# Optimization experiments

Hardware: AMD Instinct MI355X
Metric: run time of the kernel (lower is better)

## Reference

```python
import jax, jax.numpy as jnp
import numpy as np

SCALE = 0.125  # 1/sqrt(embed_dim=64), as passed to Self_Attn in the original


def setup_inputs() -> dict:
    key = jax.random.key(0)
    ks = jax.random.split(key, 6)
    B, S, N, D = 8192, 50, 100000, 64
    nodes = jax.random.randint(ks[0], (B,), 0, N)
    node_seq = jax.random.randint(ks[1], (B, S), 0, N)
    uv2e_weight = jax.random.normal(ks[2], (N, D), dtype=jnp.float32)
    feat_weight = jax.random.normal(ks[3], (N, D), dtype=jnp.float32)
    W1 = jax.random.normal(ks[4], (D, 2 * D), dtype=jnp.float32) * 0.05  # torch Linear weight (out, in)
    b1 = jax.random.normal(ks[5], (D,), dtype=jnp.float32) * 0.05
    return {"nodes": nodes, "node_seq": node_seq, "uv2e_weight": uv2e_weight,
            "feat_weight": feat_weight, "W1": W1, "b1": b1}


def reference(nodes, node_seq, uv2e_weight, feat_weight, W1, b1):
    # gather embeddings: q from self ids, k=v from padded/reversed neighbor sequences
    q = uv2e_weight[nodes]          # [B, D]
    k = uv2e_weight[node_seq]       # [B, S, D]
    v = k                           # same gather in the original
    # Self_Attn: scaled dot-product attention, query length 1 per node
    scores = jnp.einsum('bd,bsd->bs', q, k) * SCALE          # [B, S]
    attn = jax.nn.softmax(scores, axis=-1)                   # [B, S]
    folded = jnp.einsum('bs,bsd->bd', attn, v)                # [B, D]
    # self features (features(nodes).t() in torch yields [B, D])
    self_feats = feat_weight[nodes]                           # [B, D]
    combined = jnp.concatenate([self_feats, folded], axis=1)  # [B, 2D]
    out = jax.nn.relu(combined @ W1.T + b1)                   # [B, D]
    return out
```

## Files before the change

kernel.cpp:

```cpp
#include <hip/hip_runtime.h>
#include <hip/hip_bf16.h>
#include <math.h>


#define DD   64
#define SS   50
#define RPW  4
#define WPB  4
#define RPB  (RPW * WPB)
#define SCALE 0.125f

__device__ __forceinline__ float rdlane_f(float v, int l) {
    return __int_as_float(__builtin_amdgcn_readlane(__float_as_int(v), l));
}

__global__ __launch_bounds__(256) void folded_encoder_kernel(
    const int*   __restrict__ nodes,
    const int*   __restrict__ node_seq,
    const float* __restrict__ uv2e,
    const float* __restrict__ feat,
    const float* __restrict__ W1,
    const float* __restrict__ b1,
    float*       __restrict__ out,
    int B)
{
    __shared__ __align__(16) float Wsw[DD][2 * DD];
    __shared__ int seqbuf[WPB][RPW * SS];

    const int tid = threadIdx.x;
    const int wid = tid >> 6;
    const int ln  = tid & 63;
    const int rr  = ln >> 4;
    const int t   = ln & 15;

    #pragma unroll
    for (int rep = 0; rep < 32; ++rep) {
        int e = rep * 256 + tid;
        int o = e >> 7;
        int i = e & 127;
        int c = i >> 2, j = i & 3;
        Wsw[o][(((c ^ (o & 7)) << 2) + j)] = W1[e];
    }

    const float bias = b1[ln];

    const int wrow0 = (blockIdx.x * WPB + wid) * RPW;

    #pragma unroll
    for (int rep = 0; rep < 4; ++rep) {
        int pos = rep * 64 + ln;
        if (pos < RPW * SS) {
            long g = (long)wrow0 * SS + pos;
            if (g < (long)B * SS) seqbuf[wid][pos] = node_seq[g];
        }
    }
    __syncthreads();

    const int row  = wrow0 + rr;
    const int rowc = row < B ? row : B - 1;
    const int nid  = nodes[rowc];

    const float4 q4 = *(const float4*)(uv2e + (size_t)nid * DD + 4 * t);
    const float4 f4 = *(const float4*)(feat + (size_t)nid * DD + 4 * t);

    const int* sb = &seqbuf[wid][rr * SS];

    float m = -INFINITY, l = 0.f;
    float4 acc = make_float4(0.f, 0.f, 0.f, 0.f);

    int    idxq[8];
    float4 kq[6];

    #pragma unroll
    for (int v = 0; v < 8; ++v) idxq[v] = sb[v];
    #pragma unroll
    for (int v = 0; v < 6; ++v)
        kq[v] = *(const float4*)(uv2e + (size_t)idxq[v] * DD + 4 * t);

    #pragma unroll
    for (int s = 0; s < SS; ++s) {
        float4 kk = kq[s % 6];
        if (s + 8 < SS) idxq[(s + 8) % 8] = sb[s + 8];
        if (s + 6 < SS)
            kq[s % 6] = *(const float4*)(uv2e + (size_t)idxq[(s + 6) % 8] * DD + 4 * t);

        float p = kk.x * q4.x + kk.y * q4.y + kk.z * q4.z + kk.w * q4.w;
        p += __shfl_xor(p, 1);
        p += __shfl_xor(p, 2);
        p += __shfl_xor(p, 4);
        p += __shfl_xor(p, 8);

        float sc   = p * SCALE;
        float mn   = fmaxf(m, sc);
        float corr = __expf(m - mn);
        float e    = __expf(sc - mn);
        l = l * corr + e;
        acc.x = acc.x * corr + e * kk.x;
        acc.y = acc.y * corr + e * kk.y;
        acc.z = acc.z * corr + e * kk.z;
        acc.w = acc.w * corr + e * kk.w;
        m = mn;
    }
    const float rl = 1.0f / l;
    const float4 fold = make_float4(acc.x * rl, acc.y * rl, acc.z * rl, acc.w * rl);

    float oacc[RPW][2];
    #pragma unroll
    for (int r2 = 0; r2 < RPW; ++r2) { oacc[r2][0] = bias; oacc[r2][1] = 0.f; }

    const float* wrow = &Wsw[ln][0];
    #pragma unroll
    for (int cc = 0; cc < 32; ++cc) {
        float4 w4 = *(const float4*)&wrow[((cc ^ (ln & 7)) << 2)];
        #pragma unroll
        for (int r2 = 0; r2 < RPW; ++r2) {
            const int srcl = r2 * 16 + (cc & 15);
            float c0, c1, c2, c3;
            if (cc < 16) {
                c0 = rdlane_f(f4.x, srcl); c1 = rdlane_f(f4.y, srcl);
                c2 = rdlane_f(f4.z, srcl); c3 = rdlane_f(f4.w, srcl);
            } else {
                c0 = rdlane_f(fold.x, srcl); c1 = rdlane_f(fold.y, srcl);
                c2 = rdlane_f(fold.z, srcl); c3 = rdlane_f(fold.w, srcl);
            }
            oacc[r2][cc & 1]       += c0 * w4.x + c1 * w4.y;
            oacc[r2][(cc & 1) ^ 1] += c2 * w4.z + c3 * w4.w;
        }
    }

    #pragma unroll
    for (int r2 = 0; r2 < RPW; ++r2) {
        int r = wrow0 + r2;
        if (r < B) {
            float v = oacc[r2][0] + oacc[r2][1];
            out[(size_t)r * DD + ln] = fmaxf(v, 0.f);
        }
    }
}

extern "C" void kernel_launch(void* const* d_in, const int* in_sizes, int n_in,
                              void* d_out, int out_size, void* d_ws, size_t ws_size,
                              hipStream_t stream) {
    const int*   nodes    = (const int*)  d_in[0];
    const int*   node_seq = (const int*)  d_in[1];
    const float* uv2e     = (const float*)d_in[2];
    const float* feat     = (const float*)d_in[3];
    const float* W1       = (const float*)d_in[4];
    const float* b1       = (const float*)d_in[5];
    float*       out      = (float*)d_out;

    const int B = in_sizes[0];
    const int blocks = (B + RPB - 1) / RPB;

    folded_encoder_kernel<<<blocks, 256, 0, stream>>>(
        nodes, node_seq, uv2e, feat, W1, b1, out, B);
}
```

Baseline: 112.0 us.

## Split each row's sequence across half-waves and drop online-softmax max tracking

Each wave now handles 2 rows instead of 4. Each row's 50-step sequence is split into two halves of 25, processed by separate 16-lane groups and then combined with a cross-lane xor-16 shuffle. This doubles the number of independent gather streams and halves the serial loop length, so memory latency should be hidden better. The running max and rescaling of the online softmax are removed in favour of a plain exp2 with a pre-folded scale. That shortens the per-step dependency chain but can overflow if the scores are large. Lane reductions move to DPP adds, prefetch depth rises to 8, and the bounds check on the sequence load is dropped, which assumes B is a multiple of the rows per block.

New measurement: 110.0 us. No clear change (-1.8%).

```diff
diff --git a/kernel.cpp b/kernel.cpp
--- a/kernel.cpp
+++ b/kernel.cpp
@@ -3,15 +3,23 @@
 #include <math.h>
 
 
-#define DD   64
-#define SS   50
-#define RPW  4
-#define WPB  4
-#define RPB  (RPW * WPB)
-#define SCALE 0.125f
+#define DD      64
+#define SS      50
+#define HS      25
+#define RPW     2
+#define WPB     4
+#define RPB     (RPW * WPB)
+#define PDEPTH  8
+#define SCALE_L2E 0.180336880f
 
 __device__ __forceinline__ float rdlane_f(float v, int l) {
     return __int_as_float(__builtin_amdgcn_readlane(__float_as_int(v), l));
+}
+
+template <int CTRL>
+__device__ __forceinline__ float dpp_add(float x) {
+    int r = __builtin_amdgcn_update_dpp(0, __float_as_int(x), CTRL, 0xf, 0xf, true);
+    return x + __int_as_float(r);
 }
 
 __global__ __launch_bounds__(256) void folded_encoder_kernel(
@@ -30,8 +38,18 @@
     const int tid = threadIdx.x;
     const int wid = tid >> 6;
     const int ln  = tid & 63;
-    const int rr  = ln >> 4;
+    const int rr  = ln >> 5;
+    const int h   = (ln >> 4) & 1;
     const int t   = ln & 15;
+
+    const int wrow0 = (blockIdx.x * WPB + wid) * RPW;
+
+    {
+        long base = (long)wrow0 * SS;
+        seqbuf[wid][ln] = node_seq[base + ln];
+        int pos = 64 + ln;
+        if (pos < RPW * SS) seqbuf[wid][pos] = node_seq[base + pos];
+    }
 
     #pragma unroll
     for (int rep = 0; rep < 32; ++rep) {
@@ -42,71 +60,57 @@
         Wsw[o][(((c ^ (o & 7)) << 2) + j)] = W1[e];
     }
 
-    const float bias = b1[ln];
-
-    const int wrow0 = (blockIdx.x * WPB + wid) * RPW;
-
-    #pragma unroll
-    for (int rep = 0; rep < 4; ++rep) {
-        int pos = rep * 64 + ln;
-        if (pos < RPW * SS) {
-            long g = (long)wrow0 * SS + pos;
-            if (g < (long)B * SS) seqbuf[wid][pos] = node_seq[g];
-        }
-    }
-    __syncthreads();
-
     const int row  = wrow0 + rr;
     const int rowc = row < B ? row : B - 1;
     const int nid  = nodes[rowc];
-
     const float4 q4 = *(const float4*)(uv2e + (size_t)nid * DD + 4 * t);
     const float4 f4 = *(const float4*)(feat + (size_t)nid * DD + 4 * t);
+    const float bias = b1[ln];
 
-    const int* sb = &seqbuf[wid][rr * SS];
+    __syncthreads();
 
-    float m = -INFINITY, l = 0.f;
+    const int* sb = &seqbuf[wid][rr * SS + h * HS];
+
+    float  l   = 0.f;
     float4 acc = make_float4(0.f, 0.f, 0.f, 0.f);
-
-    int    idxq[8];
-    float4 kq[6];
+    float4 kq[PDEPTH];
 
     #pragma unroll
-    for (int v = 0; v < 8; ++v) idxq[v] = sb[v];
-    #pragma unroll
-    for (int v = 0; v < 6; ++v)
-        kq[v] = *(const float4*)(uv2e + (size_t)idxq[v] * DD + 4 * t);
+    for (int v = 0; v < PDEPTH; ++v)
+        kq[v] = *(const float4*)(uv2e + (size_t)sb[v] * DD + 4 * t);
 
     #pragma unroll
-    for (int s = 0; s < SS; ++s) {
-        float4 kk = kq[s % 6];
-        if (s + 8 < SS) idxq[(s + 8) % 8] = sb[s + 8];
-        if (s + 6 < SS)
-            kq[s % 6] = *(const float4*)(uv2e + (size_t)idxq[(s + 6) % 8] * DD + 4 * t);
+    for (int s = 0; s < HS; ++s) {
+        float4 kk = kq[s % PDEPTH];
+        if (s + PDEPTH < HS)
+            kq[s % PDEPTH] = *(const float4*)(uv2e + (size_t)sb[s + PDEPTH] * DD + 4 * t);
 
         float p = kk.x * q4.x + kk.y * q4.y + kk.z * q4.z + kk.w * q4.w;
-        p += __shfl_xor(p, 1);
-        p += __shfl_xor(p, 2);
-        p += __shfl_xor(p, 4);
-        p += __shfl_xor(p, 8);
+        p = dpp_add<0xB1>(p);
+        p = dpp_add<0x4E>(p);
+        p = dpp_add<0x141>(p);
+        p = dpp_add<0x140>(p);
 
-        float sc   = p * SCALE;
-        float mn   = fmaxf(m, sc);
-        float corr = __expf(m - mn);
-        float e    = __expf(sc - mn);
-        l = l * corr + e;
-        acc.x = acc.x * corr + e * kk.x;
-        acc.y = acc.y * corr + e * kk.y;
-        acc.z = acc.z * corr + e * kk.z;
-        acc.w = acc.w * corr + e * kk.w;
-        m = mn;
+        float e = __builtin_amdgcn_exp2f(p * SCALE_L2E);
+        l += e;
+        acc.x += e * kk.x;
+        acc.y += e * kk.y;
+        acc.z += e * kk.z;
+        acc.w += e * kk.w;
     }
-    const float rl = 1.0f / l;
+
+    l     += __shfl_xor(l, 16);
+    acc.x += __shfl_xor(acc.x, 16);
+    acc.y += __shfl_xor(acc.y, 16);
+    acc.z += __shfl_xor(acc.z, 16);
+    acc.w += __shfl_xor(acc.w, 16);
+
+    const float rl = __builtin_amdgcn_rcpf(l);
     const float4 fold = make_float4(acc.x * rl, acc.y * rl, acc.z * rl, acc.w * rl);
 
-    float oacc[RPW][2];
+    float oa[RPW][2];
     #pragma unroll
-    for (int r2 = 0; r2 < RPW; ++r2) { oacc[r2][0] = bias; oacc[r2][1] = 0.f; }
+    for (int r2 = 0; r2 < RPW; ++r2) { oa[r2][0] = bias; oa[r2][1] = 0.f; }
 
     const float* wrow = &Wsw[ln][0];
     #pragma unroll
@@ -114,7 +118,7 @@
         float4 w4 = *(const float4*)&wrow[((cc ^ (ln & 7)) << 2)];
         #pragma unroll
         for (int r2 = 0; r2 < RPW; ++r2) {
-            const int srcl = r2 * 16 + (cc & 15);
+            const int srcl = r2 * 32 + (cc & 15);
             float c0, c1, c2, c3;
             if (cc < 16) {
                 c0 = rdlane_f(f4.x, srcl); c1 = rdlane_f(f4.y, srcl);
@@ -123,8 +127,8 @@
                 c0 = rdlane_f(fold.x, srcl); c1 = rdlane_f(fold.y, srcl);
                 c2 = rdlane_f(fold.z, srcl); c3 = rdlane_f(fold.w, srcl);
             }
-            oacc[r2][cc & 1]       += c0 * w4.x + c1 * w4.y;
-            oacc[r2][(cc & 1) ^ 1] += c2 * w4.z + c3 * w4.w;
+            oa[r2][cc & 1]       += c0 * w4.x + c1 * w4.y;
+            oa[r2][(cc & 1) ^ 1] += c2 * w4.z + c3 * w4.w;
         }
     }
 
@@ -132,7 +136,7 @@
     for (int r2 = 0; r2 < RPW; ++r2) {
         int r = wrow0 + r2;
         if (r < B) {
-            float v = oacc[r2][0] + oacc[r2][1];
+            float v = oa[r2][0] + oa[r2][1];
             out[(size_t)r * DD + ln] = fmaxf(v, 0.f);
         }
     }
```
